# Kernel optimization log

Hardware: AMD Instinct MI355X
Metric: run time of the kernel (lower is better)

Reference implementation:

```python
import jax, jax.numpy as jnp
import numpy as np

B, Q, V, T = 96, 96, 197, 77   # image batch, text batch, visual tokens, text tokens
DV, DT, E = 768, 768, 512      # visual_size, textual_size, embed_size


def l2norm(x):
    # F.normalize(t, dim=-1, p=2) with eps=1e-12
    n = jnp.linalg.norm(x, axis=-1, keepdims=True)
    return x / jnp.maximum(n, 1e-12)


def setup_inputs() -> dict:
    key = jax.random.key(0)
    ks = jax.random.split(key, 12)
    sv = 1.0 / np.sqrt(DV).astype(np.float32)
    st = 1.0 / np.sqrt(DT).astype(np.float32)
    return {
        "visual_cls": jax.random.normal(ks[0], (B, DV), jnp.float32),
        "visual_tokens": jax.random.normal(ks[1], (B, V, DV), jnp.float32),
        "textual_cls": jax.random.normal(ks[2], (Q, DT), jnp.float32),
        "textual_tokens": jax.random.normal(ks[3], (Q, T, DT), jnp.float32),
        "Wv_cls": jax.random.normal(ks[4], (E, DV), jnp.float32) * sv,
        "bv_cls": jnp.zeros((E,), jnp.float32),
        "Wt_cls": jax.random.normal(ks[5], (E, DT), jnp.float32) * st,
        "bt_cls": jnp.zeros((E,), jnp.float32),
        "Wv_tok": jax.random.normal(ks[6], (E, DV), jnp.float32) * sv,
        "bv_tok": jnp.zeros((E,), jnp.float32),
        "Wt_tok": jax.random.normal(ks[7], (E, DT), jnp.float32) * st,
        "bt_tok": jnp.zeros((E,), jnp.float32),
        "text_length": jax.random.randint(ks[8], (Q,), 5, T + 1, jnp.int32),
    }


def reference(visual_cls, visual_tokens, textual_cls, textual_tokens,
              Wv_cls, bv_cls, Wt_cls, bt_cls,
              Wv_tok, bv_tok, Wt_tok, bt_tok, text_length):
    # Linear projections (torch nn.Linear: y = x @ W.T + b)
    v_cls = visual_cls @ Wv_cls.T + bv_cls            # [b, e]
    t_cls = textual_cls @ Wt_cls.T + bt_cls           # [q, e]
    v_tok = l2norm(jnp.einsum('bvd,ed->bve', visual_tokens, Wv_tok) + bv_tok)   # [b, v, e]
    t_tok = l2norm(jnp.einsum('qtd,ed->qte', textual_tokens, Wt_tok) + bt_tok)  # [q, t, e]

    # valid-token mask from caption lengths: mask[q, t]
    mask = (jnp.arange(T)[None, :] < text_length[:, None]).astype(v_tok.dtype)

    # fine-grained token similarity: [b, q, v, t], masked on text tokens
    logits = jnp.einsum('bve,qte->bqvt', v_tok, t_tok) * mask[None, :, None, :]

    text_sum = mask.sum(-1)                           # [q]
    t2v = logits.max(axis=2).sum(axis=2) / text_sum[None, :]   # [b, q]
    v2t = logits.max(axis=3).sum(axis=2) / V                   # [b, q]
    return (v_cls, t_cls, t2v, v2t)
```

## Files before the change

### kernel.cpp

```cpp
#include <hip/hip_runtime.h>

#define NB 96
#define NQ 96
#define NV 197
#define NT 77
#define DK 768
#define DE 512

typedef __attribute__((ext_vector_type(8))) short s16x8;
typedef __attribute__((ext_vector_type(4))) float f32x4;

__device__ __forceinline__ unsigned short f2bf(float f) {
  union { float f; unsigned int u; } v; v.f = f;
  unsigned int u = v.u;
  unsigned int r = u + 0x7fffu + ((u >> 16) & 1u);
  return (unsigned short)(r >> 16);
}

__device__ __forceinline__ unsigned int pack2bf(float a, float b) {
  return (unsigned int)f2bf(a) | ((unsigned int)f2bf(b) << 16);
}

#define GL16(gp, lp, off)                                                \
  __builtin_amdgcn_global_load_lds(                                      \
      (const __attribute__((address_space(1))) void*)(gp),               \
      (__attribute__((address_space(3))) void*)(lp), 16, (off), 0)

#define VM_DRAIN() asm volatile("s_waitcnt vmcnt(0) lgkmcnt(0)" ::: "memory")

__global__ __launch_bounds__(256) void prep_kernel(
    const float* __restrict__ Wv_tok, unsigned short* __restrict__ Wvb,
    const float* __restrict__ Wt_tok, unsigned short* __restrict__ Wtb,
    const float* __restrict__ visual_cls, const float* __restrict__ Wv_cls,
    const float* __restrict__ bv_cls, float* __restrict__ v_cls_o,
    const float* __restrict__ textual_cls, const float* __restrict__ Wt_cls,
    const float* __restrict__ bt_cls, float* __restrict__ t_cls_o) {
  __shared__ float xs[DK];
  const int blk = blockIdx.x;
  const int tid = threadIdx.x;

  if (blk < 768) {
    const float* src = (blk < 384) ? Wv_tok : Wt_tok;
    unsigned short* dst = (blk < 384) ? Wvb : Wtb;
    int i = ((blk < 384) ? blk : (blk - 384)) * 256 + tid;
    float4 x = ((const float4*)src)[i];
    ushort4 h;
    h.x = f2bf(x.x); h.y = f2bf(x.y); h.z = f2bf(x.z); h.w = f2bf(x.w);
    ((ushort4*)dst)[i] = h;
    return;
  }
  const int is_t = (blk >= 864);
  const int row = blk - (is_t ? 864 : 768);
  const float* X = is_t ? textual_cls : visual_cls;
  const float* W = is_t ? Wt_cls : Wv_cls;
  const float* bias = is_t ? bt_cls : bv_cls;
  float* out = is_t ? t_cls_o : v_cls_o;

  const float* xr = X + (long)row * DK;
  for (int i = tid; i < DK; i += 256) xs[i] = xr[i];
  __syncthreads();
  for (int c = tid; c < DE; c += 256) {
    const float* wr = W + (long)c * DK;
    float s = 0.f;
    #pragma unroll 4
    for (int k = 0; k < DK; k += 4) {
      float4 w4 = *(const float4*)(wr + k);
      s += xs[k] * w4.x + xs[k + 1] * w4.y + xs[k + 2] * w4.z + xs[k + 3] * w4.w;
    }
    out[(long)row * DE + c] = s + bias[c];
  }
}

__global__ __launch_bounds__(256, 2) void proj_norm_kernel(
    const float* __restrict__ Xv, const unsigned short* __restrict__ Wvb,
    const float* __restrict__ bv, unsigned short* __restrict__ Yv,
    const float* __restrict__ Xt, const unsigned short* __restrict__ Wtb,
    const float* __restrict__ bt, unsigned short* __restrict__ Yt) {
  __shared__ __align__(16) unsigned short Ws[512 * 64];
  __shared__ __align__(16) unsigned short Xs[64 * 64];
  __shared__ float ssq_lds[4][64];

  const int blk = blockIdx.x;
  const int is_t = (blk >= 296);
  const float* X = is_t ? Xt : Xv;
  const unsigned short* Wb = is_t ? Wtb : Wvb;
  const float* bias = is_t ? bt : bv;
  unsigned short* Y = is_t ? Yt : Yv;
  const int M = is_t ? (NQ * NT) : (NB * NV);
  const long row0 = (long)(is_t ? (blk - 296) : blk) * 64;

  const int tid = threadIdx.x;
  const int wave = tid >> 6;
  const int lane = tid & 63;
  const int l15 = lane & 15;
  const int quad = lane >> 4;

  const int sub = lane >> 3;
  const int swz = ((lane & 7) ^ sub) << 3;
  const unsigned short* pw_base = Wb + (long)(wave * 8 + sub) * DK + swz;

  const int xrow_a = tid >> 3;
  const int xrow_b = xrow_a + 32;
  const int xs8 = tid & 7;
  long gra = row0 + xrow_a; if (gra > M - 1) gra = M - 1;
  long grb = row0 + xrow_b; if (grb > M - 1) grb = M - 1;
  const float* px_a = X + gra * DK + xs8 * 8;
  const float* px_b = X + grb * DK + xs8 * 8;
  const int xaddr_a = (xrow_a << 6) + ((xs8 ^ (xrow_a & 7)) << 3);
  const int xaddr_b = (xrow_b << 6) + ((xs8 ^ (xrow_b & 7)) << 3);

  f32x4 acc[4][8];
  #pragma unroll
  for (int m = 0; m < 4; ++m)
    #pragma unroll
    for (int n = 0; n < 8; ++n)
      acc[m][n] = (f32x4){0.f, 0.f, 0.f, 0.f};

  for (int kc = 0; kc < DK; kc += 64) {
    __syncthreads();
    {
      float4 x0 = *(const float4*)(px_a);
      float4 x1 = *(const float4*)(px_a + 4);
      uint4 h;
      h.x = pack2bf(x0.x, x0.y); h.y = pack2bf(x0.z, x0.w);
      h.z = pack2bf(x1.x, x1.y); h.w = pack2bf(x1.z, x1.w);
      *(uint4*)(&Xs[xaddr_a]) = h;
      x0 = *(const float4*)(px_b);
      x1 = *(const float4*)(px_b + 4);
      h.x = pack2bf(x0.x, x0.y); h.y = pack2bf(x0.z, x0.w);
      h.z = pack2bf(x1.x, x1.y); h.w = pack2bf(x1.z, x1.w);
      *(uint4*)(&Xs[xaddr_b]) = h;
      px_a += 64; px_b += 64;
    }
    {
      const unsigned short* pw = pw_base;
      #pragma unroll
      for (int j = 0; j < 16; ++j) {
        GL16(pw, &Ws[(j * 4 + wave) << 9], 0);
        pw += 32 * DK;
      }
      pw_base += 64;
    }
    VM_DRAIN();
    __syncthreads();
    #pragma unroll
    for (int ks = 0; ks < 2; ++ks) {
      s16x8 af[4];
      #pragma unroll
      for (int mi = 0; mi < 4; ++mi) {
        int arow = mi * 16 + l15;
        af[mi] = *(const s16x8*)&Xs[(arow << 6) + ((((ks << 2) + quad) ^ (arow & 7)) << 3)];
      }
      #pragma unroll
      for (int nt = 0; nt < 8; ++nt) {
        int wrow = wave * 128 + nt * 16 + l15;
        s16x8 bfr = *(const s16x8*)&Ws[(wrow << 6) + ((((ks << 2) + quad) ^ (wrow & 7)) << 3)];
        #pragma unroll
        for (int mi = 0; mi < 4; ++mi)
          acc[mi][nt] = __builtin_amdgcn_mfma_f32_16x16x32_bf16(af[mi], bfr, acc[mi][nt], 0, 0, 0);
      }
    }
  }

  #pragma unroll
  for (int nt = 0; nt < 8; ++nt) {
    float bc = bias[wave * 128 + nt * 16 + l15];
    #pragma unroll
    for (int mi = 0; mi < 4; ++mi) {
      acc[mi][nt].x += bc; acc[mi][nt].y += bc; acc[mi][nt].z += bc; acc[mi][nt].w += bc;
    }
  }

  #pragma unroll
  for (int mi = 0; mi < 4; ++mi)
    #pragma unroll
    for (int r = 0; r < 4; ++r) {
      float t = 0.f;
      #pragma unroll
      for (int nt = 0; nt < 8; ++nt) { float v = acc[mi][nt][r]; t += v * v; }
      t += __shfl_xor(t, 1);
      t += __shfl_xor(t, 2);
      t += __shfl_xor(t, 4);
      t += __shfl_xor(t, 8);
      if (l15 == 0) ssq_lds[wave][mi * 16 + quad * 4 + r] = t;
    }
  __syncthreads();

  #pragma unroll
  for (int mi = 0; mi < 4; ++mi) {
    #pragma unroll
    for (int r = 0; r < 4; ++r) {
      int rr = mi * 16 + quad * 4 + r;
      float tot = ssq_lds[0][rr] + ssq_lds[1][rr] + ssq_lds[2][rr] + ssq_lds[3][rr];
      float scale = (tot > 0.f) ? (1.f / fmaxf(sqrtf(tot), 1e-12f)) : 0.f;
      long grow = row0 + rr;
      if (grow < M) {
        #pragma unroll
        for (int nt = 0; nt < 8; ++nt) {
          int col = wave * 128 + nt * 16 + l15;
          Y[grow * DE + col] = f2bf(acc[mi][nt][r] * scale);
        }
      }
    }
  }
}

__global__ __launch_bounds__(256, 2) void score_kernel(
    const unsigned short* __restrict__ Yv, const unsigned short* __restrict__ Yt,
    const int* __restrict__ tlen, float* __restrict__ t2v, float* __restrict__ v2t) {
  __shared__ __align__(16) unsigned short As[3][104 * 64];
  __shared__ __align__(16) unsigned short Bs[3][80 * 64];
  __shared__ float colbuf[4][160];
  __shared__ float rowsum_lds[4][2];

  const int tid = threadIdx.x;
  const int wave = tid >> 6;
  const int lane = tid & 63;
  const int l15 = lane & 15;
  const int quad = lane >> 4;

  const int idx = blockIdx.x;
  const int x = idx & 7;
  const int g = idx >> 3;
  const int qi = g / 12;
  const int bslot = g - qi * 12;
  const int b = bslot * 8 + x;
  const int q0 = qi * 2;

  const unsigned short* Ab = Yv + (long)b * (NV * DE);
  const unsigned short* Bb = Yt + (long)q0 * (NT * DE);

  {
    unsigned int* za = (unsigned int*)&As[0][0];
    for (int i = tid; i < 9984; i += 256) za[i] = 0;
    unsigned int* zb = (unsigned int*)&Bs[0][0];
    for (int i = tid; i < 7680; i += 256) zb[i] = 0;
  }
  __syncthreads();

  const int ul = lane >> 3;
  const int slot = lane & 7;
  const int kseg = ((slot >> 1) ^ (ul & 3)) << 3;

  auto a_ptr = [&](int s) -> const unsigned short* {
    int row = (s * 8 + ul) * 2 + (slot & 1);
    if (row > NV - 1) row = NV - 1;
    return Ab + row * DE + kseg;
  };
  auto b_ptr = [&](int s) -> const unsigned short* {
    int r = (s * 8 + ul) * 2 + (slot & 1);
    int half = (r >= 80) ? 1 : 0;
    int t = r - 80 * half;
    if (t > NT - 1) t = NT - 1;
    return Bb + (long)half * (NT * DE) + t * DE + kseg;
  };

  const unsigned short* sp0 = a_ptr(wave);
  const unsigned short* sp1 = a_ptr(wave + 4);
  const unsigned short* sp2 = a_ptr(wave + 8);
  const int s3 = (wave == 1) ? 8 : (wave == 2) ? 9 : 12;
  const int b3_is_b = (wave == 1 || wave == 2);
  const unsigned short* sp3 = b3_is_b ? b_ptr(s3) : a_ptr(12);
  const unsigned short* sp4 = b_ptr(wave);
  const unsigned short* sp5 = b_ptr(wave + 4);
  unsigned short* b3d0 = b3_is_b ? &Bs[0][s3 << 9] : &As[0][12 << 9];
  unsigned short* b3d1 = b3_is_b ? &Bs[1][s3 << 9] : &As[1][12 << 9];
  unsigned short* b3d2 = b3_is_b ? &Bs[2][s3 << 9] : &As[2][12 << 9];

  int aoff[4], boff[10];
  #pragma unroll
  for (int i = 0; i < 4; ++i) {
    int arow = (wave + i * 4) * 16 + l15;
    int u = arow >> 1;
    aoff[i] = (u << 6) + (((quad ^ (u & 3)) << 4)) + ((arow & 1) << 3);
  }
  #pragma unroll
  for (int nt = 0; nt < 10; ++nt) {
    int brow = nt * 16 + l15;
    int u = brow >> 1;
    boff[nt] = (u << 6) + (((quad ^ (u & 3)) << 4)) + ((brow & 1) << 3);
  }

  f32x4 acc[4][10];
  #pragma unroll
  for (int i = 0; i < 4; ++i)
    #pragma unroll
    for (int nt = 0; nt < 10; ++nt)
      acc[i][nt] = (f32x4){0.f, 0.f, 0.f, 0.f};

  auto do_compute = [&](int p) {
    s16x8 bf[10];
    #pragma unroll
    for (int nt = 0; nt < 10; ++nt)
      bf[nt] = *(const s16x8*)&Bs[p][boff[nt]];
    __builtin_amdgcn_s_setprio(1);
    #pragma unroll
    for (int i = 0; i < 4; ++i) {
      int mt = wave + (i << 2);
      if (mt < 13) {
        s16x8 af = *(const s16x8*)&As[p][aoff[i]];
        #pragma unroll
        for (int nt = 0; nt < 10; ++nt)
          acc[i][nt] = __builtin_amdgcn_mfma_f32_16x16x32_bf16(af, bf[nt], acc[i][nt], 0, 0, 0);
      }
    }
    __builtin_amdgcn_s_setprio(0);
  };

#define SCORE_STAGE(p, b3p)                                              \
  {                                                                      \
    GL16(sp0, &As[p][(wave) << 9], 0);                                   \
    GL16(sp1, &As[p][(wave + 4) << 9], 0);                               \
    GL16(sp2, &As[p][(wave + 8) << 9], 0);                               \
    GL16(sp3, (b3p), 0);                                                 \
    GL16(sp4, &Bs[p][(wave) << 9], 0);                                   \
    GL16(sp5, &Bs[p][(wave + 4) << 9], 0);                               \
    sp0 += 32; sp1 += 32; sp2 += 32; sp3 += 32; sp4 += 32; sp5 += 32;    \
  }

#define SCORE_ITER(cur, nxt, b3p, do_stage, WN)                          \
  {                                                                      \
    asm volatile("s_waitcnt vmcnt(" #WN ")" ::: "memory");               \
    __syncthreads();                                                     \
    if (do_stage) SCORE_STAGE(nxt, b3p);                                 \
    do_compute(cur);                                                     \
  }

  SCORE_STAGE(0, b3d0)
  SCORE_STAGE(1, b3d1)
  SCORE_ITER(0, 2, b3d2, 1, 6)
  SCORE_ITER(1, 0, b3d0, 1, 6)
  SCORE_ITER(2, 1, b3d1, 1, 6)
  SCORE_ITER(0, 2, b3d2, 1, 6)
  SCORE_ITER(1, 0, b3d0, 1, 6)
  SCORE_ITER(2, 1, b3d1, 1, 6)
  SCORE_ITER(0, 2, b3d2, 1, 6)
  SCORE_ITER(1, 0, b3d0, 1, 6)
  SCORE_ITER(2, 1, b3d1, 1, 6)
  SCORE_ITER(0, 2, b3d2, 1, 6)
  SCORE_ITER(1, 0, b3d0, 1, 6)
  SCORE_ITER(2, 1, b3d1, 1, 6)
  SCORE_ITER(0, 2, b3d2, 1, 6)
  SCORE_ITER(1, 0, b3d0, 1, 6)
  SCORE_ITER(2, 1, b3d1, 0, 6)
  SCORE_ITER(0, 2, b3d2, 0, 0)

#undef SCORE_ITER
#undef SCORE_STAGE

  const int len0 = tlen[q0];
  const int len1 = tlen[q0 + 1];

  #pragma unroll
  for (int nt = 0; nt < 10; ++nt) {
    float m = -1e30f;
    #pragma unroll
    for (int i = 0; i < 4; ++i) {
      int mt = wave + (i << 2);
      if (mt < 13) {
        int mbase = mt * 16 + quad * 4;
        #pragma unroll
        for (int r = 0; r < 4; ++r)
          if (mbase + r < NV) m = fmaxf(m, acc[i][nt][r]);
      }
    }
    m = fmaxf(m, __shfl_xor(m, 16));
    m = fmaxf(m, __shfl_xor(m, 32));
    if (lane < 16) colbuf[wave][nt * 16 + l15] = m;
  }

  float psum[2] = {0.f, 0.f};
  #pragma unroll
  for (int h = 0; h < 2; ++h) {
    int len = h ? len1 : len0;
    #pragma unroll
    for (int i = 0; i < 4; ++i) {
      int mt = wave + (i << 2);
      if (mt < 13) {
        int mbase = mt * 16 + quad * 4;
        #pragma unroll
        for (int r = 0; r < 4; ++r) {
          float rm = -1e30f;
          #pragma unroll
          for (int nt = 0; nt < 5; ++nt) {
            int c = nt * 16 + l15;
            if (c < len) rm = fmaxf(rm, acc[i][h * 5 + nt][r]);
          }
          rm = fmaxf(rm, __shfl_xor(rm, 1));
          rm = fmaxf(rm, __shfl_xor(rm, 2));
          rm = fmaxf(rm, __shfl_xor(rm, 4));
          rm = fmaxf(rm, __shfl_xor(rm, 8));
          if (len < NT) rm = fmaxf(rm, 0.f);
          if (l15 == 0 && (mbase + r) < NV) psum[h] += rm;
        }
      }
    }
    psum[h] += __shfl_xor(psum[h], 16);
    psum[h] += __shfl_xor(psum[h], 32);
  }
  if (lane == 0) { rowsum_lds[wave][0] = psum[0]; rowsum_lds[wave][1] = psum[1]; }
  __syncthreads();

  if (wave < 2) {
    int q = q0 + wave;
    int len = wave ? len1 : len0;
    int cbase = wave * 80;
    float ssum = 0.f;
    for (int c = lane; c < 80; c += 64) {
      if (c < len) {
        float m = fmaxf(fmaxf(colbuf[0][cbase + c], colbuf[1][cbase + c]),
                        fmaxf(colbuf[2][cbase + c], colbuf[3][cbase + c]));
        ssum += m;
      }
    }
    ssum += __shfl_xor(ssum, 1);
    ssum += __shfl_xor(ssum, 2);
    ssum += __shfl_xor(ssum, 4);
    ssum += __shfl_xor(ssum, 8);
    ssum += __shfl_xor(ssum, 16);
    ssum += __shfl_xor(ssum, 32);
    if (lane == 0) {
      float rs = rowsum_lds[0][wave] + rowsum_lds[1][wave] +
                 rowsum_lds[2][wave] + rowsum_lds[3][wave];
      t2v[b * NQ + q] = ssum / (float)len;
      v2t[b * NQ + q] = rs / (float)NV;
    }
  }
}

extern "C" void kernel_launch(void* const* d_in, const int* in_sizes, int n_in,
                              void* d_out, int out_size, void* d_ws, size_t ws_size,
                              hipStream_t stream) {
  (void)in_sizes; (void)n_in; (void)out_size; (void)ws_size;
  const float* visual_cls     = (const float*)d_in[0];
  const float* visual_tokens  = (const float*)d_in[1];
  const float* textual_cls    = (const float*)d_in[2];
  const float* textual_tokens = (const float*)d_in[3];
  const float* Wv_cls = (const float*)d_in[4];
  const float* bv_cls = (const float*)d_in[5];
  const float* Wt_cls = (const float*)d_in[6];
  const float* bt_cls = (const float*)d_in[7];
  const float* Wv_tok = (const float*)d_in[8];
  const float* bv_tok = (const float*)d_in[9];
  const float* Wt_tok = (const float*)d_in[10];
  const float* bt_tok = (const float*)d_in[11];
  const int* text_length = (const int*)d_in[12];

  float* out = (float*)d_out;
  float* v_cls_o = out;
  float* t_cls_o = out + 49152;
  float* t2v_o   = out + 98304;
  float* v2t_o   = out + 107520;

  char* ws = (char*)d_ws;
  unsigned short* Wvb = (unsigned short*)(ws);
  unsigned short* Wtb = (unsigned short*)(ws + 786432);
  unsigned short* Yv  = (unsigned short*)(ws + 1572864);
  unsigned short* Yt  = (unsigned short*)(ws + 20938752);

  prep_kernel<<<960, 256, 0, stream>>>(
      Wv_tok, Wvb, Wt_tok, Wtb,
      visual_cls, Wv_cls, bv_cls, v_cls_o,
      textual_cls, Wt_cls, bt_cls, t_cls_o);

  proj_norm_kernel<<<412, 256, 0, stream>>>(
      visual_tokens, Wvb, bv_tok, Yv,
      textual_tokens, Wtb, bt_tok, Yt);

  score_kernel<<<(NB * NQ) / 2, 256, 0, stream>>>(Yv, Yt, text_length, t2v_o, v2t_o);
}
```

Measured before the change: 447.0 us.

## Store normalized token embeddings as FP8 and use FP8 MFMA in score kernel

The projection kernel now writes the normalized token embeddings as FP8 E4M3 bytes through a software converter instead of bf16, which halves the intermediate buffers. The score kernel loads 64-byte K chunks per stage, runs 16x16x32 fp8 MFMAs in two k-substeps, and needs half as many pipeline iterations. This targets global traffic and MFMA throughput in the dominant similarity GEMM. It lowers precision of the logits, which could affect the max/sum results within tolerance.

```diff
diff --git a/kernel.cpp b/kernel.cpp
--- a/kernel.cpp
+++ b/kernel.cpp
@@ -9,6 +9,7 @@
 
 typedef __attribute__((ext_vector_type(8))) short s16x8;
 typedef __attribute__((ext_vector_type(4))) float f32x4;
+typedef long long i64;
 
 __device__ __forceinline__ unsigned short f2bf(float f) {
   union { float f; unsigned int u; } v; v.f = f;
@@ -19,6 +20,24 @@
 
 __device__ __forceinline__ unsigned int pack2bf(float a, float b) {
   return (unsigned int)f2bf(a) | ((unsigned int)f2bf(b) << 16);
+}
+
+__device__ __forceinline__ unsigned char f2fp8(float x) {
+  union { float f; unsigned u; } v; v.f = x;
+  unsigned s = (v.u >> 24) & 0x80;
+  v.u &= 0x7FFFFFFFu;
+  if (v.f < 0.015625f) {
+    int q = __float2int_rn(v.f * 512.0f);
+    return (unsigned char)(s | (unsigned)q);
+  }
+  if (v.f >= 464.0f) return (unsigned char)(s | 0x7E);
+  int e8 = (int)((v.u >> 23) & 0xFF) - 120;
+  unsigned m = v.u & 0x7FFFFFu;
+  unsigned t = ((unsigned)e8 << 3) | (m >> 20);
+  unsigned r = m & 0xFFFFFu;
+  t += (r > 0x80000u) || ((r == 0x80000u) && (t & 1u));
+  if (t > 0x7Eu) t = 0x7Eu;
+  return (unsigned char)(s | t);
 }
 
 #define GL16(gp, lp, off)                                                \
@@ -73,9 +92,9 @@
 
 __global__ __launch_bounds__(256, 2) void proj_norm_kernel(
     const float* __restrict__ Xv, const unsigned short* __restrict__ Wvb,
-    const float* __restrict__ bv, unsigned short* __restrict__ Yv,
+    const float* __restrict__ bv, unsigned char* __restrict__ Yv,
     const float* __restrict__ Xt, const unsigned short* __restrict__ Wtb,
-    const float* __restrict__ bt, unsigned short* __restrict__ Yt) {
+    const float* __restrict__ bt, unsigned char* __restrict__ Yt) {
   __shared__ __align__(16) unsigned short Ws[512 * 64];
   __shared__ __align__(16) unsigned short Xs[64 * 64];
   __shared__ float ssq_lds[4][64];
@@ -85,7 +104,7 @@
   const float* X = is_t ? Xt : Xv;
   const unsigned short* Wb = is_t ? Wtb : Wvb;
   const float* bias = is_t ? bt : bv;
-  unsigned short* Y = is_t ? Yt : Yv;
+  unsigned char* Y = is_t ? Yt : Yv;
   const int M = is_t ? (NQ * NT) : (NB * NV);
   const long row0 = (long)(is_t ? (blk - 296) : blk) * 64;
 
@@ -198,7 +217,7 @@
         #pragma unroll
         for (int nt = 0; nt < 8; ++nt) {
           int col = wave * 128 + nt * 16 + l15;
-          Y[grow * DE + col] = f2bf(acc[mi][nt][r] * scale);
+          Y[grow * DE + col] = f2fp8(acc[mi][nt][r] * scale);
         }
       }
     }
@@ -206,10 +225,10 @@
 }
 
 __global__ __launch_bounds__(256, 2) void score_kernel(
-    const unsigned short* __restrict__ Yv, const unsigned short* __restrict__ Yt,
+    const unsigned char* __restrict__ Yv, const unsigned char* __restrict__ Yt,
     const int* __restrict__ tlen, float* __restrict__ t2v, float* __restrict__ v2t) {
-  __shared__ __align__(16) unsigned short As[3][104 * 64];
-  __shared__ __align__(16) unsigned short Bs[3][80 * 64];
+  __shared__ __align__(16) unsigned char As[3][104 * 128];
+  __shared__ __align__(16) unsigned char Bs[3][80 * 128];
   __shared__ float colbuf[4][160];
   __shared__ float rowsum_lds[4][2];
 
@@ -227,8 +246,8 @@
   const int b = bslot * 8 + x;
   const int q0 = qi * 2;
 
-  const unsigned short* Ab = Yv + (long)b * (NV * DE);
-  const unsigned short* Bb = Yt + (long)q0 * (NT * DE);
+  const unsigned char* Ab = Yv + (long)b * (NV * DE);
+  const unsigned char* Bb = Yt + (long)q0 * (NT * DE);
 
   {
     unsigned int* za = (unsigned int*)&As[0][0];
@@ -240,45 +259,47 @@
 
   const int ul = lane >> 3;
   const int slot = lane & 7;
-  const int kseg = ((slot >> 1) ^ (ul & 3)) << 3;
-
-  auto a_ptr = [&](int s) -> const unsigned short* {
+  const int kq16 = (((slot >> 1) ^ (ul & 3)) << 4);
+
+  auto a_ptr = [&](int s) -> const unsigned char* {
     int row = (s * 8 + ul) * 2 + (slot & 1);
     if (row > NV - 1) row = NV - 1;
-    return Ab + row * DE + kseg;
+    return Ab + row * DE + kq16;
   };
-  auto b_ptr = [&](int s) -> const unsigned short* {
+  auto b_ptr = [&](int s) -> const unsigned char* {
     int r = (s * 8 + ul) * 2 + (slot & 1);
     int half = (r >= 80) ? 1 : 0;
     int t = r - 80 * half;
     if (t > NT - 1) t = NT - 1;
-    return Bb + (long)half * (NT * DE) + t * DE + kseg;
+    return Bb + (long)half * (NT * DE) + t * DE + kq16;
   };
 
-  const unsigned short* sp0 = a_ptr(wave);
-  const unsigned short* sp1 = a_ptr(wave + 4);
-  const unsigned short* sp2 = a_ptr(wave + 8);
+  const unsigned char* sp0 = a_ptr(wave);
+  const unsigned char* sp1 = a_ptr(wave + 4);
+  const unsigned char* sp2 = a_ptr(wave + 8);
   const int s3 = (wave == 1) ? 8 : (wave == 2) ? 9 : 12;
   const int b3_is_b = (wave == 1 || wave == 2);
-  const unsigned short* sp3 = b3_is_b ? b_ptr(s3) : a_ptr(12);
-  const unsigned short* sp4 = b_ptr(wave);
-  const unsigned short* sp5 = b_ptr(wave + 4);
-  unsigned short* b3d0 = b3_is_b ? &Bs[0][s3 << 9] : &As[0][12 << 9];
-  unsigned short* b3d1 = b3_is_b ? &Bs[1][s3 << 9] : &As[1][12 << 9];
-  unsigned short* b3d2 = b3_is_b ? &Bs[2][s3 << 9] : &As[2][12 << 9];
-
+  const unsigned char* sp3 = b3_is_b ? b_ptr(s3) : a_ptr(12);
+  const unsigned char* sp4 = b_ptr(wave);
+  const unsigned char* sp5 = b_ptr(wave + 4);
+  unsigned char* b3d0 = b3_is_b ? &Bs[0][s3 << 10] : &As[0][12 << 10];
+  unsigned char* b3d1 = b3_is_b ? &Bs[1][s3 << 10] : &As[1][12 << 10];
+  unsigned char* b3d2 = b3_is_b ? &Bs[2][s3 << 10] : &As[2][12 << 10];
+
+  const int qh = quad >> 1;
+  const int q8 = (quad & 1) << 3;
   int aoff[4], boff[10];
   #pragma unroll
   for (int i = 0; i < 4; ++i) {
     int arow = (wave + i * 4) * 16 + l15;
     int u = arow >> 1;
-    aoff[i] = (u << 6) + (((quad ^ (u & 3)) << 4)) + ((arow & 1) << 3);
+    aoff[i] = (u << 7) + (((qh ^ (u & 3))) << 5) + ((arow & 1) << 4) + q8;
   }
   #pragma unroll
   for (int nt = 0; nt < 10; ++nt) {
     int brow = nt * 16 + l15;
     int u = brow >> 1;
-    boff[nt] = (u << 6) + (((quad ^ (u & 3)) << 4)) + ((brow & 1) << 3);
+    boff[nt] = (u << 7) + (((qh ^ (u & 3))) << 5) + ((brow & 1) << 4) + q8;
   }
 
   f32x4 acc[4][10];
@@ -289,33 +310,37 @@
       acc[i][nt] = (f32x4){0.f, 0.f, 0.f, 0.f};
 
   auto do_compute = [&](int p) {
-    s16x8 bf[10];
-    #pragma unroll
-    for (int nt = 0; nt < 10; ++nt)
-      bf[nt] = *(const s16x8*)&Bs[p][boff[nt]];
-    __builtin_amdgcn_s_setprio(1);
-    #pragma unroll
-    for (int i = 0; i < 4; ++i) {
-      int mt = wave + (i << 2);
-      if (mt < 13) {
-        s16x8 af = *(const s16x8*)&As[p][aoff[i]];
-        #pragma unroll
-        for (int nt = 0; nt < 10; ++nt)
-          acc[i][nt] = __builtin_amdgcn_mfma_f32_16x16x32_bf16(af, bf[nt], acc[i][nt], 0, 0, 0);
-      }
-    }
-    __builtin_amdgcn_s_setprio(0);
+    #pragma unroll
+    for (int ks = 0; ks < 2; ++ks) {
+      const int kx = ks ? 64 : 0;
+      i64 bf[10];
+      #pragma unroll
+      for (int nt = 0; nt < 10; ++nt)
+        bf[nt] = *(const i64*)&Bs[p][boff[nt] ^ kx];
+      __builtin_amdgcn_s_setprio(1);
+      #pragma unroll
+      for (int i = 0; i < 4; ++i) {
+        int mt = wave + (i << 2);
+        if (mt < 13) {
+          i64 af = *(const i64*)&As[p][aoff[i] ^ kx];
+          #pragma unroll
+          for (int nt = 0; nt < 10; ++nt)
+            acc[i][nt] = __builtin_amdgcn_mfma_f32_16x16x32_fp8_fp8(af, bf[nt], acc[i][nt], 0, 0, 0);
+        }
+      }
+      __builtin_amdgcn_s_setprio(0);
+    }
   };
 
 #define SCORE_STAGE(p, b3p)                                              \
   {                                                                      \
-    GL16(sp0, &As[p][(wave) << 9], 0);                                   \
-    GL16(sp1, &As[p][(wave + 4) << 9], 0);                               \
-    GL16(sp2, &As[p][(wave + 8) << 9], 0);                               \
+    GL16(sp0, &As[p][(wave) << 10], 0);                                  \
+    GL16(sp1, &As[p][(wave + 4) << 10], 0);                              \
+    GL16(sp2, &As[p][(wave + 8) << 10], 0);                              \
     GL16(sp3, (b3p), 0);                                                 \
-    GL16(sp4, &Bs[p][(wave) << 9], 0);                                   \
-    GL16(sp5, &Bs[p][(wave + 4) << 9], 0);                               \
-    sp0 += 32; sp1 += 32; sp2 += 32; sp3 += 32; sp4 += 32; sp5 += 32;    \
+    GL16(sp4, &Bs[p][(wave) << 10], 0);                                  \
+    GL16(sp5, &Bs[p][(wave + 4) << 10], 0);                              \
+    sp0 += 64; sp1 += 64; sp2 += 64; sp3 += 64; sp4 += 64; sp5 += 64;    \
   }
 
 #define SCORE_ITER(cur, nxt, b3p, do_stage, WN)                          \
@@ -334,16 +359,8 @@
   SCORE_ITER(0, 2, b3d2, 1, 6)
   SCORE_ITER(1, 0, b3d0, 1, 6)
   SCORE_ITER(2, 1, b3d1, 1, 6)
-  SCORE_ITER(0, 2, b3d2, 1, 6)
-  SCORE_ITER(1, 0, b3d0, 1, 6)
-  SCORE_ITER(2, 1, b3d1, 1, 6)
-  SCORE_ITER(0, 2, b3d2, 1, 6)
-  SCORE_ITER(1, 0, b3d0, 1, 6)
-  SCORE_ITER(2, 1, b3d1, 1, 6)
-  SCORE_ITER(0, 2, b3d2, 1, 6)
-  SCORE_ITER(1, 0, b3d0, 1, 6)
-  SCORE_ITER(2, 1, b3d1, 0, 6)
-  SCORE_ITER(0, 2, b3d2, 0, 0)
+  SCORE_ITER(0, 2, b3d2, 0, 6)
+  SCORE_ITER(1, 0, b3d0, 0, 0)
 
 #undef SCORE_ITER
 #undef SCORE_STAGE
@@ -455,8 +472,8 @@
   char* ws = (char*)d_ws;
   unsigned short* Wvb = (unsigned short*)(ws);
   unsigned short* Wtb = (unsigned short*)(ws + 786432);
-  unsigned short* Yv  = (unsigned short*)(ws + 1572864);
-  unsigned short* Yt  = (unsigned short*)(ws + 20938752);
+  unsigned char*  Yv  = (unsigned char*)(ws + 1572864);
+  unsigned char*  Yt  = (unsigned char*)(ws + 1572864 + 9683968);
 
   prep_kernel<<<960, 256, 0, stream>>>(
       Wv_tok, Wvb, Wt_tok, Wtb,
```

After: 416.3 us. -6.9%, faster.
